# Performance work log

Hardware: AMD Instinct MI355X
Metric: run time of the kernel (lower is better)

The kernel has to match this reference:

```python
import jax, jax.numpy as jnp
import numpy as np

D = 2048; H = 8; HD = 256; KV = 4; GHD = 512; GKV = 4; ROT = 128
F = 8192; V = 32000; B = 2; S = 1024; WIN = 512; EPS = 1e-6
THETA_S = 10000.0; THETA_G = 1000000.0


def _rms(x, w):
    return x * jax.lax.rsqrt(jnp.mean(x * x, axis=-1, keepdims=True) + EPS) * w


def _rms_ns(x):
    return x * jax.lax.rsqrt(jnp.mean(x * x, axis=-1, keepdims=True) + EPS)


def _angles(d, theta):
    # cos/sin tables: [S, d//2]
    inv = 1.0 / (theta ** (jnp.arange(0, d, 2, dtype=jnp.float32) / d))
    ang = jnp.arange(S, dtype=jnp.float32)[:, None] * inv[None, :]
    return jnp.cos(ang), jnp.sin(ang)


def _rope(x, cos, sin):
    # x: [B,S,H,d]; interleaved complex rotation on pairs
    b, s, h, d = x.shape
    xr = x.reshape(b, s, h, d // 2, 2)
    x1, x2 = xr[..., 0], xr[..., 1]
    c = cos[None, :, None, :]
    sn = sin[None, :, None, :]
    return jnp.stack([x1 * c - x2 * sn, x1 * sn + x2 * c], axis=-1).reshape(b, s, h, d)


def _partial_rope(x, cos, sin, rot):
    if rot == x.shape[-1]:
        return _rope(x, cos, sin)
    return jnp.concatenate([_rope(x[..., :rot], cos, sin), x[..., rot:]], axis=-1)


def _block(x, wq, wk, wv, wo, qn, kn, wg, wu, wd, ln1, ln2, ln3, ln4, scal,
           cos, sin, rot, mask, n_rep):
    res = x
    h = _rms(x, ln1)
    xq = jnp.einsum('bsd,dhc->bshc', h, wq)
    xk = jnp.einsum('bsd,dkc->bskc', h, wk)
    if wv is None:
        xv = _rms_ns(xk)  # global block: V = unscaled-RMS-normed K (pre k_norm)
    else:
        xv = _rms_ns(jnp.einsum('bsd,dkc->bskc', h, wv))
    xq = _rms(xq, qn)
    xk = _rms(xk, kn)
    xq = _partial_rope(xq, cos, sin, rot)
    xk = _partial_rope(xk, cos, sin, rot)
    q = xq.transpose(0, 2, 1, 3)  # [B,H,S,d]
    k = xk.transpose(0, 2, 1, 3)
    v = xv.transpose(0, 2, 1, 3)
    if n_rep != 1:
        k = jnp.repeat(k, n_rep, axis=1)
        v = jnp.repeat(v, n_rep, axis=1)
    scores = jnp.einsum('bhqd,bhkd->bhqk', q, k)  # NOTE: no 1/sqrt(d), as in source
    p = jax.nn.softmax(scores.astype(jnp.float32), axis=-1, where=mask[:, None, :, :]).astype(x.dtype)
    o = jnp.einsum('bhqk,bhkd->bhqd', p, v).transpose(0, 2, 1, 3)
    o = o.reshape(x.shape[0], x.shape[1], -1)
    o = _rms(jnp.einsum('bsd,do->bso', o, wo), ln2)
    x = res + o
    res = x
    hf = _rms(x, ln3)
    ffn = jnp.einsum('bsf,fd->bsd',
                     jax.nn.gelu(jnp.einsum('bsd,df->bsf', hf, wg), approximate=True)
                     * jnp.einsum('bsd,df->bsf', hf, wu), wd)
    x = res + _rms(ffn, ln4)
    return x * scal


def setup_inputs() -> dict:
    key = jax.random.key(0)
    ks = jax.random.split(key, 20)
    n = lambda k, shp: jax.random.normal(k, shp, jnp.float32) * 0.02
    inp = {
        'tokens': jax.random.randint(ks[0], (B, S), 0, V, jnp.int32),
        'true_lengths': jnp.full((B,), S, jnp.int32),
        'embed': n(ks[1], (V, D)),
        'norm_w': jnp.ones((D,), jnp.float32),
        's_wq': n(ks[2], (D, H, HD)), 's_wk': n(ks[3], (D, KV, HD)), 's_wv': n(ks[4], (D, KV, HD)),
        's_wo': n(ks[5], (H * HD, D)),
        's_qn': jnp.ones((HD,), jnp.float32), 's_kn': jnp.ones((HD,), jnp.float32),
        's_wg': n(ks[6], (D, F)), 's_wu': n(ks[7], (D, F)), 's_wd': n(ks[8], (F, D)),
        's_ln1': jnp.ones((D,), jnp.float32), 's_ln2': jnp.ones((D,), jnp.float32),
        's_ln3': jnp.ones((D,), jnp.float32), 's_ln4': jnp.ones((D,), jnp.float32),
        's_scal': jnp.ones((1,), jnp.float32),
        'g_wq': n(ks[9], (D, H, GHD)), 'g_wk': n(ks[10], (D, GKV, GHD)),
        'g_wo': n(ks[11], (H * GHD, D)),
        'g_qn': jnp.ones((GHD,), jnp.float32), 'g_kn': jnp.ones((GHD,), jnp.float32),
        'g_wg': n(ks[12], (D, F)), 'g_wu': n(ks[13], (D, F)), 'g_wd': n(ks[14], (F, D)),
        'g_ln1': jnp.ones((D,), jnp.float32), 'g_ln2': jnp.ones((D,), jnp.float32),
        'g_ln3': jnp.ones((D,), jnp.float32), 'g_ln4': jnp.ones((D,), jnp.float32),
        'g_scal': jnp.ones((1,), jnp.float32),
    }
    return inp


def reference(tokens, true_lengths, embed, norm_w,
              s_wq, s_wk, s_wv, s_wo, s_qn, s_kn, s_wg, s_wu, s_wd,
              s_ln1, s_ln2, s_ln3, s_ln4, s_scal,
              g_wq, g_wk, g_wo, g_qn, g_kn, g_wg, g_wu, g_wd,
              g_ln1, g_ln2, g_ln3, g_ln4, g_scal):
    # prefill from empty cache: seq_positions = 0, cache len == seqlen
    qpos = jnp.arange(S)[:, None]
    kpos = jnp.arange(S)[None, :]
    causal = qpos >= kpos
    sw = causal & ((qpos - kpos) < WIN)
    kvalid = kpos[None, 0, :][None, :] if False else (jnp.arange(S)[None, :] < true_lengths[:, None])  # [B,S]
    sliding_mask = sw[None, :, :] & kvalid[:, None, :]
    global_mask = causal[None, :, :] & kvalid[:, None, :]

    cos_s, sin_s = _angles(HD, THETA_S)
    cos_g, sin_g = _angles(ROT, THETA_G)

    h = embed[tokens] * jnp.sqrt(jnp.float32(D))
    h = _block(h, s_wq, s_wk, s_wv, s_wo, s_qn, s_kn, s_wg, s_wu, s_wd,
               s_ln1, s_ln2, s_ln3, s_ln4, s_scal, cos_s, sin_s, HD, sliding_mask, H // KV)
    h = _block(h, g_wq, g_wk, None, g_wo, g_qn, g_kn, g_wg, g_wu, g_wd,
               g_ln1, g_ln2, g_ln3, g_ln4, g_scal, cos_g, sin_g, ROT, global_mask, H // GKV)
    h = _rms(h, norm_w)
    logits = jnp.einsum('bsd,vd->bsv', h, embed)  # tied embedding head
    return logits
```

## Files before the change

kernel.cpp:

```cpp
#include <hip/hip_runtime.h>
#include <math.h>

typedef unsigned short u16;
typedef _Float16 f16;
typedef __attribute__((ext_vector_type(8))) _Float16 f16x8;
typedef __attribute__((ext_vector_type(4))) float f32x4;

constexpr int cB   = 2;
constexpr int cS   = 1024;
constexpr int cD   = 2048;
constexpr int cH   = 8;
constexpr int cHD  = 256;
constexpr int cKV  = 4;
constexpr int cGHD = 512;
constexpr int cGKV = 4;
constexpr int cROT = 128;
constexpr int cF   = 8192;
constexpr int cV   = 32000;
constexpr int cWIN = 512;
constexpr int cM   = cB * cS;
constexpr float cEPS = 1e-6f;
constexpr size_t MB = 1024 * 1024;

__device__ inline u16 f2h(float x) { union { f16 h; u16 u; } c; c.h = (f16)x; return c.u; }
__device__ inline float h2f(u16 v) { union { u16 u; f16 h; } c; c.u = v; return (float)c.h; }

__device__ inline int swz16(int row, int chunk) {
    return row * 32 + ((chunk ^ ((row >> 1) & 3)) << 3);
}
__device__ inline int swzK(int row, int ch) {
    return row * 64 + ((ch ^ (row & 7)) << 3);
}

typedef __attribute__((address_space(1))) const unsigned int gu32;
typedef __attribute__((address_space(3))) unsigned int lu32;
__device__ inline void ldsload16(const u16* g, u16* l) {
    __builtin_amdgcn_global_load_lds((gu32*)g, (lu32*)l, 16, 0, 0);
}

__device__ inline float gelu_tanh(float v) {
    const float t = tanhf(0.7978845608028654f * (v + 0.044715f * v * v * v));
    return 0.5f * v * (1.f + t);
}

__global__ void embed_kernel(const int* __restrict__ tok,
                             const float* __restrict__ emb,
                             float* __restrict__ out) {
    const int row = blockIdx.x;
    const int t = tok[row];
    const float* e = emb + (size_t)t * cD;
    float* o = out + (size_t)row * cD;
    const float sc = sqrtf((float)cD);
    for (int d = threadIdx.x; d < cD; d += blockDim.x) o[d] = e[d] * sc;
}

__global__ void rms_kernel(const float* __restrict__ x,
                           const float* __restrict__ w,
                           float* __restrict__ out, int dim, int xld, int nh) {
    const int row = blockIdx.x;
    const float* xr = x + (size_t)(row / nh) * xld + (size_t)(row % nh) * dim;
    float* orow = out + (size_t)row * dim;
    float ss = 0.f;
    for (int d = threadIdx.x; d < dim; d += blockDim.x) { float v = xr[d]; ss += v * v; }
    for (int o = 32; o >= 1; o >>= 1) ss += __shfl_xor(ss, o);
    __shared__ float rb[8];
    if ((threadIdx.x & 63) == 0) rb[threadIdx.x >> 6] = ss;
    __syncthreads();
    ss = rb[0] + rb[1] + rb[2] + rb[3];
    const float r = rsqrtf(ss / dim + cEPS);
    for (int d = threadIdx.x; d < dim; d += blockDim.x)
        orow[d] = xr[d] * r * (w ? w[d] : 1.f);
}

__global__ void rms_f16_kernel(const float* __restrict__ x,
                               const float* __restrict__ w,
                               u16* __restrict__ out, int dim) {
    const int row = blockIdx.x;
    const float* xr = x + (size_t)row * dim;
    u16* orow = out + (size_t)row * dim;
    float ss = 0.f;
    for (int d = threadIdx.x; d < dim; d += blockDim.x) { float v = xr[d]; ss += v * v; }
    for (int o = 32; o >= 1; o >>= 1) ss += __shfl_xor(ss, o);
    __shared__ float rb[8];
    if ((threadIdx.x & 63) == 0) rb[threadIdx.x >> 6] = ss;
    __syncthreads();
    ss = rb[0] + rb[1] + rb[2] + rb[3];
    const float r = rsqrtf(ss / dim + cEPS);
    for (int d = threadIdx.x; d < dim; d += blockDim.x)
        orow[d] = f2h(xr[d] * r * (w ? w[d] : 1.f));
}

__global__ __launch_bounds__(256) void addnorm_kernel(const float* __restrict__ res,
                                                      const float* __restrict__ y,
                                                      const float* __restrict__ w_add,
                                                      const float* __restrict__ scal,
                                                      const float* __restrict__ w_norm,
                                                      float* __restrict__ xout,
                                                      u16* __restrict__ abo) {
    const int row = blockIdx.x;
    const float* yr = y + (size_t)row * cD;
    const float* rr = res + (size_t)row * cD;
    float* xo = xout + (size_t)row * cD;
    u16* ao = abo + (size_t)row * cD;
    const int tid = threadIdx.x;
    __shared__ float rb[4];

    float yl[8], xl[8];
    float ss = 0.f;
#pragma unroll
    for (int j = 0; j < 8; ++j) { yl[j] = yr[tid + j * 256]; ss += yl[j] * yl[j]; }
    for (int o = 32; o >= 1; o >>= 1) ss += __shfl_xor(ss, o);
    if ((tid & 63) == 0) rb[tid >> 6] = ss;
    __syncthreads();
    ss = rb[0] + rb[1] + rb[2] + rb[3];
    const float r1 = rsqrtf(ss / cD + cEPS);
    const float sc = scal ? *scal : 1.f;

    float ss2 = 0.f;
#pragma unroll
    for (int j = 0; j < 8; ++j) {
        const int d = tid + j * 256;
        xl[j] = (rr[d] + yl[j] * r1 * w_add[d]) * sc;
        ss2 += xl[j] * xl[j];
    }
    for (int o = 32; o >= 1; o >>= 1) ss2 += __shfl_xor(ss2, o);
    __syncthreads();
    if ((tid & 63) == 0) rb[tid >> 6] = ss2;
    __syncthreads();
    ss2 = rb[0] + rb[1] + rb[2] + rb[3];
    const float r2 = rsqrtf(ss2 / cD + cEPS);
#pragma unroll
    for (int j = 0; j < 8; ++j) {
        const int d = tid + j * 256;
        xo[d] = xl[j];
        ao[d] = f2h(xl[j] * r2 * w_norm[d]);
    }
}

__global__ __launch_bounds__(128) void rmsrope_kernel(const float* __restrict__ x,
                                                      const float* __restrict__ w,
                                                      u16* __restrict__ out,
                                                      int NH, int HDIM, int rot,
                                                      float theta, int xld) {
    const int row = blockIdx.x;
    const int s = (row / NH) % cS;
    const float* xr = x + (size_t)(row / NH) * xld + (size_t)(row % NH) * HDIM;
    u16* orow = out + (size_t)row * HDIM;
    const int tid = threadIdx.x;
    const int np = HDIM >> 1;
    __shared__ float rb[2];

    float v1[2], v2[2];
    float ss = 0.f;
    for (int p = tid, j = 0; p < np; p += 128, ++j) {
        v1[j] = xr[2 * p]; v2[j] = xr[2 * p + 1];
        ss += v1[j] * v1[j] + v2[j] * v2[j];
    }
    for (int o = 32; o >= 1; o >>= 1) ss += __shfl_xor(ss, o);
    if ((tid & 63) == 0) rb[tid >> 6] = ss;
    __syncthreads();
    ss = rb[0] + rb[1];
    const float r = rsqrtf(ss / HDIM + cEPS);
    const int halfrot = rot >> 1;
    for (int p = tid, j = 0; p < np; p += 128, ++j) {
        const float a = v1[j] * r * w[2 * p];
        const float b = v2[j] * r * w[2 * p + 1];
        float o1 = a, o2 = b;
        if (p < halfrot) {
            const float inv = powf(theta, -(2.f * p) / (float)rot);
            const float ang = (float)s * inv;
            const float c = cosf(ang), sn = sinf(ang);
            o1 = a * c - b * sn;
            o2 = a * sn + b * c;
        }
        orow[2 * p]     = f2h(o1);
        orow[2 * p + 1] = f2h(o2);
    }
}

__global__ __launch_bounds__(256) void tcast_kernel(const float* __restrict__ in,
                                                    u16* __restrict__ out,
                                                    int K, int N, int ldin) {
    __shared__ float t[32][33];
    const int kt = blockIdx.y * 32, nt = blockIdx.x * 32;
    const int tx = threadIdx.x & 31, ty = threadIdx.x >> 5;
#pragma unroll
    for (int j = 0; j < 4; ++j)
        t[ty + j * 8][tx] = in[(size_t)(kt + ty + j * 8) * ldin + nt + tx];
    __syncthreads();
#pragma unroll
    for (int j = 0; j < 4; ++j)
        out[(size_t)(nt + ty + j * 8) * K + kt + tx] = f2h(t[tx][ty + j * 8]);
}

__global__ void cast_f16_kernel(const float* __restrict__ in, u16* __restrict__ out,
                                int n) {
    const int i = blockIdx.x * blockDim.x + threadIdx.x;
    if (i * 4 >= n) return;
    const float4 v = *(const float4*)&in[(size_t)i * 4];
    uint2 o;
    o.x = (unsigned)f2h(v.x) | ((unsigned)f2h(v.y) << 16);
    o.y = (unsigned)f2h(v.z) | ((unsigned)f2h(v.w) << 16);
    *(uint2*)&out[(size_t)i * 4] = o;
}

__global__ __launch_bounds__(256) void vtrans_kernel(const float* __restrict__ V,
                                                     u16* __restrict__ Vt,
                                                     int HDIM, int KVH) {
    __shared__ float t[32][33];
    const int bk = blockIdx.z;
    const int b = bk / KVH, kh = bk % KVH;
    const int st = blockIdx.y * 32, dt = blockIdx.x * 32;
    const int tx = threadIdx.x & 31, ty = threadIdx.x >> 5;
#pragma unroll
    for (int j = 0; j < 4; ++j)
        t[ty + j * 8][tx] = V[((size_t)(b * cS + st + ty + j * 8) * KVH + kh) * HDIM + dt + tx];
    __syncthreads();
#pragma unroll
    for (int j = 0; j < 4; ++j)
        Vt[((size_t)bk * HDIM + dt + ty + j * 8) * cS + st + tx] = f2h(t[tx][ty + j * 8]);
}

template<bool F16_OUT, bool GELU>
__global__ __launch_bounds__(256) void gemm_f16(const u16* __restrict__ A,
                                                const u16* __restrict__ Bt,
                                                void* __restrict__ Cout,
                                                const u16* __restrict__ gate,
                                                int Mt, int K, int ldc) {
    __shared__ u16 As[128 * 32];
    __shared__ u16 Bs[128 * 32];
    const int nwg = gridDim.x;
    const int q8 = nwg >> 3;
    const int dd = blockIdx.x;
    const int wk = (dd & 7) * q8 + (dd >> 3);
    const int bm = (wk % Mt) * 128;
    const int bn = (wk / Mt) * 128;
    const int tid = threadIdx.x;
    const int lane = tid & 63;
    const int wv = tid >> 6;
    const int wr = (wv >> 1) * 64, wc = (wv & 1) * 64;
    const int r15 = lane & 15, hi16 = lane >> 4;

    f32x4 acc[4][4];
#pragma unroll
    for (int m = 0; m < 4; ++m)
#pragma unroll
        for (int n = 0; n < 4; ++n) acc[m][n] = (f32x4){0.f, 0.f, 0.f, 0.f};

    int rowS[2], koS[2];
#pragma unroll
    for (int i = 0; i < 2; ++i) {
        const int s = i * 256 + tid;
        rowS[i] = s >> 2;
        koS[i] = ((s & 3) ^ ((rowS[i] >> 1) & 3)) * 8;
    }
    u16* ldsA0 = &As[(wv * 64) * 8];
    u16* ldsA1 = &As[(256 + wv * 64) * 8];
    u16* ldsB0 = &Bs[(wv * 64) * 8];
    u16* ldsB1 = &Bs[(256 + wv * 64) * 8];

    for (int k0 = 0; k0 < K; k0 += 32) {
        __syncthreads();
        ldsload16(&A [(size_t)(bm + rowS[0]) * K + k0 + koS[0]], ldsA0);
        ldsload16(&A [(size_t)(bm + rowS[1]) * K + k0 + koS[1]], ldsA1);
        ldsload16(&Bt[(size_t)(bn + rowS[0]) * K + k0 + koS[0]], ldsB0);
        ldsload16(&Bt[(size_t)(bn + rowS[1]) * K + k0 + koS[1]], ldsB1);
        __syncthreads();
        f16x8 af[4], bf4[4];
#pragma unroll
        for (int m = 0; m < 4; ++m)
            af[m] = *(const f16x8*)&As[swz16(wr + m * 16 + r15, hi16)];
#pragma unroll
        for (int n = 0; n < 4; ++n)
            bf4[n] = *(const f16x8*)&Bs[swz16(wc + n * 16 + r15, hi16)];
#pragma unroll
        for (int m = 0; m < 4; ++m)
#pragma unroll
            for (int n = 0; n < 4; ++n)
                acc[m][n] = __builtin_amdgcn_mfma_f32_16x16x32_f16(af[m], bf4[n], acc[m][n], 0, 0, 0);
    }
#pragma unroll
    for (int m = 0; m < 4; ++m)
#pragma unroll
        for (int n = 0; n < 4; ++n)
#pragma unroll
            for (int r = 0; r < 4; ++r) {
                const int row = bm + wr + m * 16 + hi16 * 4 + r;
                const int col = bn + wc + n * 16 + r15;
                const size_t idx = (size_t)row * ldc + col;
                float v = acc[m][n][r];
                if (GELU) v = gelu_tanh(h2f(gate[idx])) * v;
                if (F16_OUT) ((u16*)Cout)[idx] = f2h(v);
                else         ((float*)Cout)[idx] = v;
            }
}

template<bool F16_OUT, bool GELU>
__global__ __launch_bounds__(512) void gemm256(const u16* __restrict__ A,
                                               const u16* __restrict__ Bt,
                                               void* __restrict__ Cout,
                                               const u16* __restrict__ gate,
                                               int Mt, int K, int ldc) {
    __shared__ u16 As[2][256 * 64];
    __shared__ u16 Bs[2][256 * 64];
    const int nwg = gridDim.x;
    const int q8 = nwg >> 3;
    const int dd = blockIdx.x;
    const int wk = (dd & 7) * q8 + (dd >> 3);
    const int bm = (wk % Mt) * 256;
    const int bn = (wk / Mt) * 256;
    const int tid = threadIdx.x;
    const int lane = tid & 63;
    const int wid = tid >> 6;
    const int wm = wid >> 2, wn = wid & 3;
    const int r15 = lane & 15, hi16 = lane >> 4;

    f32x4 acc[8][4];
#pragma unroll
    for (int mi = 0; mi < 8; ++mi)
#pragma unroll
        for (int ni = 0; ni < 4; ++ni) acc[mi][ni] = (f32x4){0.f, 0.f, 0.f, 0.f};

    const int rl = lane >> 3;
    const int sch = ((lane & 7) ^ rl) * 8;
    const int srow = wid * 32 + rl;

    const int nt = K / 64;

#pragma unroll
    for (int i = 0; i < 4; ++i) {
        ldsload16(&A [(size_t)(bm + srow + i * 8) * K + sch], &As[0][(wid * 32 + i * 8) * 64]);
        ldsload16(&Bt[(size_t)(bn + srow + i * 8) * K + sch], &Bs[0][(wid * 32 + i * 8) * 64]);
    }
    __syncthreads();

    for (int t = 0; t < nt; ++t) {
        const int cur = t & 1;
        if (t + 1 < nt) {
            const int nb = cur ^ 1;
            const size_t k0 = (size_t)(t + 1) * 64 + sch;
#pragma unroll
            for (int i = 0; i < 4; ++i) {
                ldsload16(&A [(size_t)(bm + srow + i * 8) * K + k0], &As[nb][(wid * 32 + i * 8) * 64]);
                ldsload16(&Bt[(size_t)(bn + srow + i * 8) * K + k0], &Bs[nb][(wid * 32 + i * 8) * 64]);
            }
        }
        const u16* Ab = As[cur];
        const u16* Bb = Bs[cur];
#pragma unroll
        for (int kk = 0; kk < 2; ++kk) {
            f16x8 bf[4], af[8];
#pragma unroll
            for (int ni = 0; ni < 4; ++ni)
                bf[ni] = *(const f16x8*)&Bb[swzK(wn * 64 + ni * 16 + r15, kk * 4 + hi16)];
#pragma unroll
            for (int mi = 0; mi < 8; ++mi)
                af[mi] = *(const f16x8*)&Ab[swzK(wm * 128 + mi * 16 + r15, kk * 4 + hi16)];
            __builtin_amdgcn_s_setprio(1);
#pragma unroll
            for (int mi = 0; mi < 8; ++mi)
#pragma unroll
                for (int ni = 0; ni < 4; ++ni)
                    acc[mi][ni] = __builtin_amdgcn_mfma_f32_16x16x32_f16(af[mi], bf[ni], acc[mi][ni], 0, 0, 0);
            __builtin_amdgcn_s_setprio(0);
        }
        __syncthreads();
    }

#pragma unroll
    for (int mi = 0; mi < 8; ++mi)
#pragma unroll
        for (int ni = 0; ni < 4; ++ni)
#pragma unroll
            for (int r = 0; r < 4; ++r) {
                const int row = bm + wm * 128 + mi * 16 + hi16 * 4 + r;
                const int col = bn + wn * 64 + ni * 16 + r15;
                const size_t idx = (size_t)row * ldc + col;
                float v = acc[mi][ni][r];
                if (GELU) v = gelu_tanh(h2f(gate[idx])) * v;
                if (F16_OUT) ((u16*)Cout)[idx] = f2h(v);
                else         ((float*)Cout)[idx] = v;
            }
}

__global__ __launch_bounds__(256) void qk_f16(const u16* __restrict__ Qh,
                                              const u16* __restrict__ Kh,
                                              float* __restrict__ Sc,
                                              int HDIM, int KVH, int win) {
    const int bm = blockIdx.y * 128;
    const int bn = blockIdx.x * 128;
    if (bn > bm + 127) return;
    if (win > 0 && bm - bn > win + 126) return;
    const int bh = blockIdx.z;
    const int b = bh / cH, h = bh % cH;
    const int kh = h / (cH / KVH);

    __shared__ u16 As[128 * 64];
    __shared__ u16 Bs[128 * 64];
    const int tid = threadIdx.x;
    const int lane = tid & 63;
    const int w = tid >> 6;
    const int wr = (w >> 1) * 64, wc = (w & 1) * 64;
    const int r15 = lane & 15, hi16 = lane >> 4;

    const int lda = cH * HDIM, ldb = KVH * HDIM;
    const u16* Aq = Qh + ((size_t)b * cS * cH + h) * HDIM;
    const u16* Bk = Kh + ((size_t)b * cS * KVH + kh) * HDIM;

    f32x4 acc[4][4];
#pragma unroll
    for (int m = 0; m < 4; ++m)
#pragma unroll
        for (int n = 0; n < 4; ++n) acc[m][n] = (f32x4){0.f, 0.f, 0.f, 0.f};

    int rA[4], cA[4], wl[4];
#pragma unroll
    for (int j = 0; j < 4; ++j) {
        const int c = tid + j * 256;
        rA[j] = c >> 3; cA[j] = (c & 7) * 8;
        wl[j] = swzK(rA[j], c & 7);
    }

    for (int k0 = 0; k0 < HDIM; k0 += 64) {
        uint4 av[4], bv[4];
#pragma unroll
        for (int j = 0; j < 4; ++j) {
            av[j] = *(const uint4*)&Aq[(size_t)(bm + rA[j]) * lda + k0 + cA[j]];
            bv[j] = *(const uint4*)&Bk[(size_t)(bn + rA[j]) * ldb + k0 + cA[j]];
        }
        __syncthreads();
#pragma unroll
        for (int j = 0; j < 4; ++j) {
            *(uint4*)&As[wl[j]] = av[j];
            *(uint4*)&Bs[wl[j]] = bv[j];
        }
        __syncthreads();
#pragma unroll
        for (int kk = 0; kk < 2; ++kk) {
            f16x8 af[4], bf4[4];
#pragma unroll
            for (int m = 0; m < 4; ++m)
                af[m] = *(const f16x8*)&As[swzK(wr + m * 16 + r15, kk * 4 + hi16)];
#pragma unroll
            for (int n = 0; n < 4; ++n)
                bf4[n] = *(const f16x8*)&Bs[swzK(wc + n * 16 + r15, kk * 4 + hi16)];
#pragma unroll
            for (int m = 0; m < 4; ++m)
#pragma unroll
                for (int n = 0; n < 4; ++n)
                    acc[m][n] = __builtin_amdgcn_mfma_f32_16x16x32_f16(af[m], bf4[n], acc[m][n], 0, 0, 0);
        }
    }
    float* Crow = Sc + (size_t)bh * cS * cS;
#pragma unroll
    for (int m = 0; m < 4; ++m)
#pragma unroll
        for (int n = 0; n < 4; ++n)
#pragma unroll
            for (int r = 0; r < 4; ++r)
                Crow[(size_t)(bm + wr + m * 16 + hi16 * 4 + r) * cS + bn + wc + n * 16 + r15]
                    = acc[m][n][r];
}

__global__ __launch_bounds__(256) void softmax_kernel(float* __restrict__ Sc,
                                                      const int* __restrict__ tlen,
                                                      int win) {
    const int q = blockIdx.x, bh = blockIdx.y, b = bh / cH;
    float* row = Sc + ((size_t)bh * cS + q) * cS;
    u16* rowh = (u16*)row;
    const int tid = threadIdx.x;
    const int tl = tlen[b];
    const int kmax = min(q, tl - 1);
    const int kmin = (win > 0) ? max(0, q - win + 1) : 0;

    float v[4];
    float m = -1e30f;
#pragma unroll
    for (int j = 0; j < 4; ++j) {
        const int k = tid + j * 256;
        const bool ok = (k >= kmin && k <= kmax);
        v[j] = ok ? row[k] : -1e30f;
        m = fmaxf(m, v[j]);
    }
    for (int o = 32; o >= 1; o >>= 1) m = fmaxf(m, __shfl_xor(m, o));
    __shared__ float rb[8];
    if ((tid & 63) == 0) rb[tid >> 6] = m;
    __syncthreads();
    m = fmaxf(fmaxf(rb[0], rb[1]), fmaxf(rb[2], rb[3]));

    float e[4];
    float s = 0.f;
#pragma unroll
    for (int j = 0; j < 4; ++j) {
        const int k = tid + j * 256;
        const bool ok = (k >= kmin && k <= kmax);
        e[j] = ok ? expf(v[j] - m) : 0.f;
        s += e[j];
    }
    for (int o = 32; o >= 1; o >>= 1) s += __shfl_xor(s, o);
    __shared__ float sb[4];
    if ((tid & 63) == 0) sb[tid >> 6] = s;
    __syncthreads();
    s = sb[0] + sb[1] + sb[2] + sb[3];
    const float inv = 1.f / s;
    __syncthreads();
#pragma unroll
    for (int j = 0; j < 4; ++j) {
        const int k = tid + j * 256;
        rowh[k] = f2h(e[j] * inv);
    }
}

__global__ __launch_bounds__(256) void pv_f16(const u16* __restrict__ P,
                                              const u16* __restrict__ Vt,
                                              u16* __restrict__ O,
                                              int HDIM, int KVH, int win) {
    const int bh = blockIdx.z;
    const int b = bh / cH, h = bh % cH;
    const int kh = h / (cH / KVH);
    const int bm = blockIdx.y * 128;
    const int bn = blockIdx.x * 128;

    __shared__ u16 As[128 * 64];
    __shared__ u16 Bs[128 * 64];
    const int tid = threadIdx.x;
    const int lane = tid & 63;
    const int w = tid >> 6;
    const int wr = (w >> 1) * 64, wc = (w & 1) * 64;
    const int r15 = lane & 15, hi16 = lane >> 4;

    const u16* Ap = P + (size_t)bh * cS * 2048;
    const u16* Bv = Vt + ((size_t)b * KVH + kh) * HDIM * cS;

    f32x4 acc[4][4];
#pragma unroll
    for (int m = 0; m < 4; ++m)
#pragma unroll
        for (int n = 0; n < 4; ++n) acc[m][n] = (f32x4){0.f, 0.f, 0.f, 0.f};

    int rA[4], cA[4], wl[4];
#pragma unroll
    for (int j = 0; j < 4; ++j) {
        const int c = tid + j * 256;
        rA[j] = c >> 3; cA[j] = (c & 7) * 8;
        wl[j] = swzK(rA[j], c & 7);
    }

    const int klo = (win > 0) ? (max(0, bm - win + 1) & ~63) : 0;
    const int khi = min(bm + 128, cS);

    for (int k0 = klo; k0 < khi; k0 += 64) {
        uint4 av[4], bv[4];
#pragma unroll
        for (int j = 0; j < 4; ++j) {
            av[j] = *(const uint4*)&Ap[(size_t)(bm + rA[j]) * 2048 + k0 + cA[j]];
            bv[j] = *(const uint4*)&Bv[(size_t)(bn + rA[j]) * cS + k0 + cA[j]];
        }
        __syncthreads();
#pragma unroll
        for (int j = 0; j < 4; ++j) {
            *(uint4*)&As[wl[j]] = av[j];
            *(uint4*)&Bs[wl[j]] = bv[j];
        }
        __syncthreads();
#pragma unroll
        for (int kk = 0; kk < 2; ++kk) {
            f16x8 af[4], bf4[4];
#pragma unroll
            for (int m = 0; m < 4; ++m)
                af[m] = *(const f16x8*)&As[swzK(wr + m * 16 + r15, kk * 4 + hi16)];
#pragma unroll
            for (int n = 0; n < 4; ++n)
                bf4[n] = *(const f16x8*)&Bs[swzK(wc + n * 16 + r15, kk * 4 + hi16)];
#pragma unroll
            for (int m = 0; m < 4; ++m)
#pragma unroll
                for (int n = 0; n < 4; ++n)
                    acc[m][n] = __builtin_amdgcn_mfma_f32_16x16x32_f16(af[m], bf4[n], acc[m][n], 0, 0, 0);
        }
    }
    const int ldo = cH * HDIM;
#pragma unroll
    for (int m = 0; m < 4; ++m)
#pragma unroll
        for (int n = 0; n < 4; ++n)
#pragma unroll
            for (int r = 0; r < 4; ++r) {
                const int q = bm + wr + m * 16 + hi16 * 4 + r;
                const int d = bn + wc + n * 16 + r15;
                O[(size_t)(b * cS + q) * ldo + h * HDIM + d] = f2h(acc[m][n][r]);
            }
}

extern "C" void kernel_launch(void* const* d_in, const int* in_sizes, int n_in,
                              void* d_out, int out_size, void* d_ws, size_t ws_size,
                              hipStream_t stream) {
    (void)in_sizes; (void)n_in; (void)out_size; (void)ws_size;
    const int*   tokens = (const int*)  d_in[0];
    const int*   tlen   = (const int*)  d_in[1];
    const float* embed  = (const float*)d_in[2];
    const float* norm_w = (const float*)d_in[3];
    const float* s_wq   = (const float*)d_in[4];
    const float* s_wk   = (const float*)d_in[5];
    const float* s_wv   = (const float*)d_in[6];
    const float* s_wo   = (const float*)d_in[7];
    const float* s_qn   = (const float*)d_in[8];
    const float* s_kn   = (const float*)d_in[9];
    const float* s_wg   = (const float*)d_in[10];
    const float* s_wu   = (const float*)d_in[11];
    const float* s_wd   = (const float*)d_in[12];
    const float* s_ln1  = (const float*)d_in[13];
    const float* s_ln2  = (const float*)d_in[14];
    const float* s_ln3  = (const float*)d_in[15];
    const float* s_ln4  = (const float*)d_in[16];
    const float* s_scal = (const float*)d_in[17];
    const float* g_wq   = (const float*)d_in[18];
    const float* g_wk   = (const float*)d_in[19];
    const float* g_wo   = (const float*)d_in[20];
    const float* g_qn   = (const float*)d_in[21];
    const float* g_kn   = (const float*)d_in[22];
    const float* g_wg   = (const float*)d_in[23];
    const float* g_wu   = (const float*)d_in[24];
    const float* g_wd   = (const float*)d_in[25];
    const float* g_ln1  = (const float*)d_in[26];
    const float* g_ln2  = (const float*)d_in[27];
    const float* g_ln3  = (const float*)d_in[28];
    const float* g_ln4  = (const float*)d_in[29];
    const float* g_scal = (const float*)d_in[30];

    char* w8 = (char*)d_ws;
    float* x   = (float*)(w8);
    u16*   ab  = (u16*)(w8 + 16 * MB);
    u16*   wp  = (u16*)(w8 + 24 * MB);
    u16*   Qb  = (u16*)(w8 + 24 * MB);
    u16*   Ob  = (u16*)(w8 + 24 * MB);
    u16*   embH= (u16*)(w8 + 24 * MB);
    u16*   t0b = (u16*)(w8 + 56 * MB);
    u16*   Kb  = (u16*)(w8 + 58 * MB);
    u16*   Vt  = (u16*)(w8 + 75 * MB);
    float* qkg = (float*)(w8 + 84 * MB);
    float* scores = (float*)(w8 + 84 * MB);
    u16*   Pb  = (u16*)(w8 + 84 * MB);
    u16*   wo2 = (u16*)(w8 + 84 * MB);
    u16*   t1b = (u16*)(w8 + 88 * MB);
    float* r0  = (float*)(w8 + 116 * MB);
    float* fo  = (float*)(w8 + 120 * MB);
    float* vf  = (float*)(w8 + 132 * MB);

    auto tcast = [&](const float* in, u16* outp, int K, int N, int ldin) {
        tcast_kernel<<<dim3(N / 32, K / 32), 256, 0, stream>>>(in, outp, K, N, ldin);
    };
    auto gemmF = [&](const u16* A, const u16* Bt, float* C, int N, int K, int ldc) {
        gemm_f16<false, false><<<16 * (N / 128), 256, 0, stream>>>(A, Bt, C, nullptr, 16, K, ldc);
    };
    auto g256H = [&](const u16* A, const u16* Bt, u16* C, int N, int K, int ldc) {
        gemm256<true, false><<<8 * (N / 256), 512, 0, stream>>>(A, Bt, C, nullptr, 8, K, ldc);
    };
    auto g256HG = [&](const u16* A, const u16* Bt, u16* C, const u16* gate,
                      int N, int K, int ldc) {
        gemm256<true, true><<<8 * (N / 256), 512, 0, stream>>>(A, Bt, C, gate, 8, K, ldc);
    };

    auto attention = [&](int HDIM, int KVH, int win) {
        vtrans_kernel<<<dim3(HDIM / 32, cS / 32, cB * KVH), 256, 0, stream>>>(vf, Vt, HDIM, KVH);
        qk_f16<<<dim3(cS / 128, cS / 128, cB * cH), 256, 0, stream>>>(
            Qb, Kb, scores, HDIM, KVH, win);
        softmax_kernel<<<dim3(cS, cB * cH), 256, 0, stream>>>(scores, tlen, win);
        pv_f16<<<dim3(HDIM / 128, cS / 128, cB * cH), 256, 0, stream>>>(
            Pb, Vt, Ob, HDIM, KVH, win);
    };

    embed_kernel<<<cM, 256, 0, stream>>>(tokens, embed, x);

    rms_f16_kernel<<<cM, 256, 0, stream>>>(x, s_ln1, ab, cD);
    tcast(s_wq, wp, cD, cH * cHD, cH * cHD);
    tcast(s_wk, wp + (size_t)2048 * cD, cD, cKV * cHD, cKV * cHD);
    tcast(s_wv, wp + (size_t)3072 * cD, cD, cKV * cHD, cKV * cHD);
    gemmF(ab, wp, qkg, 4096, cD, 4096);
    rms_kernel<<<cM * cKV, 256, 0, stream>>>(qkg + 3072, nullptr, vf, cHD, 4096, cKV);
    rmsrope_kernel<<<cM * cH, 128, 0, stream>>>(qkg, s_qn, Qb, cH, cHD, cHD, 10000.f, 4096);
    rmsrope_kernel<<<cM * cKV, 128, 0, stream>>>(qkg + 2048, s_kn, Kb, cKV, cHD, cHD, 10000.f, 4096);
    attention(cHD, cKV, cWIN);
    tcast(s_wo, wo2, cH * cHD, cD, cD);
    gemmF(Ob, wo2, r0, cD, cH * cHD, cD);
    addnorm_kernel<<<cM, 256, 0, stream>>>(x, r0, s_ln2, nullptr, s_ln3, x, ab);
    tcast(s_wg, wp, cD, cF, cF);
    g256H(ab, wp, t1b, cF, cD, cF);
    tcast(s_wu, wp, cD, cF, cF);
    g256HG(ab, wp, t0b, t1b, cF, cD, cF);
    tcast(s_wd, wp, cF, cD, cD);
    gemmF(t0b, wp, fo, cD, cF, cD);
    addnorm_kernel<<<cM, 256, 0, stream>>>(x, fo, s_ln4, s_scal, g_ln1, x, ab);

    tcast(g_wq, wp, cD, cH * cGHD, cH * cGHD);
    tcast(g_wk, wp + (size_t)4096 * cD, cD, cGKV * cGHD, cGKV * cGHD);
    gemmF(ab, wp, qkg, 6144, cD, 6144);
    rms_kernel<<<cM * cGKV, 256, 0, stream>>>(qkg + 4096, nullptr, vf, cGHD, 6144, cGKV);
    rmsrope_kernel<<<cM * cH, 128, 0, stream>>>(qkg, g_qn, Qb, cH, cGHD, cROT, 1000000.f, 6144);
    rmsrope_kernel<<<cM * cGKV, 128, 0, stream>>>(qkg + 4096, g_kn, Kb, cGKV, cGHD, cROT, 1000000.f, 6144);
    attention(cGHD, cGKV, 0);
    tcast(g_wo, wo2, cH * cGHD, cD, cD);
    gemmF(Ob, wo2, r0, cD, cH * cGHD, cD);
    addnorm_kernel<<<cM, 256, 0, stream>>>(x, r0, g_ln2, nullptr, g_ln3, x, ab);
    tcast(g_wg, wp, cD, cF, cF);
    g256H(ab, wp, t1b, cF, cD, cF);
    tcast(g_wu, wp, cD, cF, cF);
    g256HG(ab, wp, t0b, t1b, cF, cD, cF);
    tcast(g_wd, wp, cF, cD, cD);
    gemmF(t0b, wp, fo, cD, cF, cD);
    addnorm_kernel<<<cM, 256, 0, stream>>>(x, fo, g_ln4, g_scal, norm_w, x, ab);

    cast_f16_kernel<<<(cV * cD / 4 + 255) / 256, 256, 0, stream>>>(embed, embH, cV * cD);
    gemm256<false, false><<<8 * (cV / 256), 512, 0, stream>>>(
        ab, embH, (float*)d_out, nullptr, 8, cD, cV);
}
```

Before: 1.936 ms.

## Triple-buffer gemm256 LDS staging with BK=32 and explicit vmcnt waits

Replaces the double-buffered BK=64 staging in the 256x256 GEMM with a three-stage ring of BK=32 tiles. Loads are issued two tiles ahead, and exact s_waitcnt vmcnt counts are used instead of a full __syncthreads drain. A new pair-row XOR swizzle packs two 32-wide rows per 64-element LDS line. The goal is to keep more global loads in flight and to cut LDS usage, in exchange for twice as many barrier rounds per K and a hand-tuned wait count that must match the number of loads per stage.

```diff
diff --git a/kernel.cpp b/kernel.cpp
--- a/kernel.cpp
+++ b/kernel.cpp
@@ -301,8 +301,8 @@
                                                void* __restrict__ Cout,
                                                const u16* __restrict__ gate,
                                                int Mt, int K, int ldc) {
-    __shared__ u16 As[2][256 * 64];
-    __shared__ u16 Bs[2][256 * 64];
+    __shared__ u16 As[3][256 * 32];
+    __shared__ u16 Bs[3][256 * 32];
     const int nwg = gridDim.x;
     const int q8 = nwg >> 3;
     const int dd = blockIdx.x;
@@ -321,50 +321,63 @@
 #pragma unroll
         for (int ni = 0; ni < 4; ++ni) acc[mi][ni] = (f32x4){0.f, 0.f, 0.f, 0.f};
 
-    const int rl = lane >> 3;
-    const int sch = ((lane & 7) ^ rl) * 8;
-    const int srow = wid * 32 + rl;
-
-    const int nt = K / 64;
-
-#pragma unroll
-    for (int i = 0; i < 4; ++i) {
-        ldsload16(&A [(size_t)(bm + srow + i * 8) * K + sch], &As[0][(wid * 32 + i * 8) * 64]);
-        ldsload16(&Bt[(size_t)(bn + srow + i * 8) * K + sch], &Bs[0][(wid * 32 + i * 8) * 64]);
-    }
-    __syncthreads();
-
+    const int rpl  = lane >> 3;
+    const int ch8d = (lane & 7) ^ rpl;
+    const int sr   = wid * 16 + rpl * 2 + (ch8d >> 2);
+    const int sk   = (ch8d & 3) * 8;
+    const int ldst = wid * 512;
+
+    auto stage = [&](int t, int b) {
+        const size_t k0 = (size_t)t * 32 + sk;
+        ldsload16(&A [(size_t)(bm + sr)       * K + k0], &As[b][ldst]);
+        ldsload16(&A [(size_t)(bm + 128 + sr) * K + k0], &As[b][4096 + ldst]);
+        ldsload16(&Bt[(size_t)(bn + sr)       * K + k0], &Bs[b][ldst]);
+        ldsload16(&Bt[(size_t)(bn + 128 + sr) * K + k0], &Bs[b][4096 + ldst]);
+    };
+
+    const int nt = K / 32;
+    stage(0, 0);
+    stage(1, 1);
+    int cur = 0, nxt2 = 2;
     for (int t = 0; t < nt; ++t) {
-        const int cur = t & 1;
-        if (t + 1 < nt) {
-            const int nb = cur ^ 1;
-            const size_t k0 = (size_t)(t + 1) * 64 + sch;
-#pragma unroll
-            for (int i = 0; i < 4; ++i) {
-                ldsload16(&A [(size_t)(bm + srow + i * 8) * K + k0], &As[nb][(wid * 32 + i * 8) * 64]);
-                ldsload16(&Bt[(size_t)(bn + srow + i * 8) * K + k0], &Bs[nb][(wid * 32 + i * 8) * 64]);
-            }
-        }
+        if (t + 2 < nt) {
+            stage(t + 2, nxt2);
+            asm volatile("s_waitcnt vmcnt(8)" ::: "memory");
+        } else if (t + 1 < nt) {
+            asm volatile("s_waitcnt vmcnt(4)" ::: "memory");
+        } else {
+            asm volatile("s_waitcnt vmcnt(0)" ::: "memory");
+        }
+        __builtin_amdgcn_s_barrier();
+        __builtin_amdgcn_sched_barrier(0);
         const u16* Ab = As[cur];
         const u16* Bb = Bs[cur];
-#pragma unroll
-        for (int kk = 0; kk < 2; ++kk) {
-            f16x8 bf[4], af[8];
+        f16x8 bf[4], af[8];
+#pragma unroll
+        for (int ni = 0; ni < 4; ++ni) {
+            const int row = wn * 64 + ni * 16 + r15;
+            const int rp = row >> 1;
+            const int slot = (((row & 1) << 2) | hi16) ^ (rp & 7);
+            bf[ni] = *(const f16x8*)&Bb[rp * 64 + slot * 8];
+        }
+#pragma unroll
+        for (int mi = 0; mi < 8; ++mi) {
+            const int row = wm * 128 + mi * 16 + r15;
+            const int rp = row >> 1;
+            const int slot = (((row & 1) << 2) | hi16) ^ (rp & 7);
+            af[mi] = *(const f16x8*)&Ab[rp * 64 + slot * 8];
+        }
+        __builtin_amdgcn_s_setprio(1);
+#pragma unroll
+        for (int mi = 0; mi < 8; ++mi)
 #pragma unroll
             for (int ni = 0; ni < 4; ++ni)
-                bf[ni] = *(const f16x8*)&Bb[swzK(wn * 64 + ni * 16 + r15, kk * 4 + hi16)];
-#pragma unroll
-            for (int mi = 0; mi < 8; ++mi)
-                af[mi] = *(const f16x8*)&Ab[swzK(wm * 128 + mi * 16 + r15, kk * 4 + hi16)];
-            __builtin_amdgcn_s_setprio(1);
-#pragma unroll
-            for (int mi = 0; mi < 8; ++mi)
-#pragma unroll
-                for (int ni = 0; ni < 4; ++ni)
-                    acc[mi][ni] = __builtin_amdgcn_mfma_f32_16x16x32_f16(af[mi], bf[ni], acc[mi][ni], 0, 0, 0);
-            __builtin_amdgcn_s_setprio(0);
-        }
-        __syncthreads();
+                acc[mi][ni] = __builtin_amdgcn_mfma_f32_16x16x32_f16(af[mi], bf[ni], acc[mi][ni], 0, 0, 0);
+        __builtin_amdgcn_s_setprio(0);
+        __builtin_amdgcn_sched_barrier(0);
+        __builtin_amdgcn_s_barrier();
+        cur = nxt2 - 1; if (cur < 0) cur = 2;
+        nxt2 = nxt2 + 1; if (nxt2 == 3) nxt2 = 0;
     }
 
 #pragma unroll
```

Measured after the change: 2.029 ms. +4.8%, slower.
